# Kernel optimization log

Measured on AMD Instinct MI355X. Metric: run time of the kernel, lower is better.

Reference implementation:

```python
import jax, jax.numpy as jnp
import numpy as np
import math


def ste_round(x):
    # round with straight-through gradient (identity in bwd)
    return x + jax.lax.stop_gradient(jnp.round(x) - x)


def ste_floor(x):
    return x + jax.lax.stop_gradient(jnp.floor(x) - x)


def _conv(x, w, b):
    # 5x5 stride-2 conv, padding=2 (kernel_size//2), NCHW/OIHW
    y = jax.lax.conv_general_dilated(
        x, w, window_strides=(2, 2), padding=[(2, 2), (2, 2)],
        dimension_numbers=('NCHW', 'OIHW', 'NCHW'))
    return y + b[None, :, None, None]


def _split_conv(x, w, b_int, mul, split=4):
    # 4 redundant sub-convolutions with floor-STE quantized integer weights/biases
    wq = ste_round(w)  # wSTE: round-to-int with STE
    out = 0.0
    for i in range(split):
        out = out + _conv(x, ste_floor((wq + i) / split), ste_floor((b_int + i) / split))
    return out * mul[None, :, None, None]


def _forward(x, w0, b0, w1, b1, w2, b2, w3, b3, mul0, mul1, mul2, mul3,
             relu0, relu1, relu2, md0, md1, md2, md3, ga_left):
    Bits = 8; clp_k = 8; in_scale = 8; scl_k = 3
    relus = [relu0, relu1, relu2]
    clp = [round((2 ** Bits - 1) / r * 2 ** (16 + clp_k)) for r in relus]
    scl = [math.floor((r + 2 ** (scl_k - 1)) / 2 ** scl_k) for r in relus]

    # quantize input to uint8 range
    x = jnp.clip(ste_round(x * 2 ** in_scale), 0, 255)

    # ---- layer 0 ----
    x = _split_conv(x, w0, ste_round(b0 * 2 ** in_scale), mul0)
    x = ste_floor((x + 2.0 ** (md0 - 1 + in_scale - clp_k)) / 2.0 ** (md0 + in_scale - clp_k))
    x = jnp.clip(x, 0, clp[0])
    x = ste_floor((ste_round(x * scl[0]) + 2.0 ** (15 + clp_k - scl_k)) / 2.0 ** (16 + clp_k - scl_k))

    # ---- layers 1, 2 ----
    for w_, b_, mul_, md_, idx in ((w1, b1, mul1, md1, 1), (w2, b2, mul2, md2, 2)):
        x = _split_conv(x, w_, ste_round(b_), mul_)
        x = ste_floor((x + 2.0 ** (md_ - 1 - clp_k)) / 2.0 ** (md_ - clp_k))
        x = jnp.clip(x, 0, clp[idx])
        x = ste_floor((ste_round(x * scl[idx]) + 2.0 ** (15 + clp_k - scl_k)) / 2.0 ** (16 + clp_k - scl_k))

    # ---- layer 3 (latent) ----
    x = _split_conv(x, w3, ste_round(b3), mul3)
    x = ste_floor((x + 2.0 ** (md3 - 1 - ga_left)) / 2.0 ** (md3 - ga_left))
    return x


def setup_inputs():
    key = jax.random.key(0)
    ks = jax.random.split(key, 16)
    N, M = 192, 320
    d = {}
    d['x'] = jax.random.uniform(ks[0], (4, 3, 512, 512), dtype=jnp.float32)
    # float weights whose round() gives small ints (integerized LIC weights)
    d['w0'] = jax.random.normal(ks[1], (N, 3, 5, 5), dtype=jnp.float32) * 3.0
    d['b0'] = jax.random.normal(ks[2], (N,), dtype=jnp.float32)
    d['w1'] = jax.random.normal(ks[3], (N, N, 5, 5), dtype=jnp.float32) * 3.0
    d['b1'] = jax.random.normal(ks[4], (N,), dtype=jnp.float32) * 16.0
    d['w2'] = jax.random.normal(ks[5], (N, N, 5, 5), dtype=jnp.float32) * 3.0
    d['b2'] = jax.random.normal(ks[6], (N,), dtype=jnp.float32) * 16.0
    d['w3'] = jax.random.normal(ks[7], (M, N, 5, 5), dtype=jnp.float32) * 3.0
    d['b3'] = jax.random.normal(ks[8], (M,), dtype=jnp.float32) * 16.0
    # per-channel integer-valued fixed-point multipliers
    d['mul0'] = jax.random.randint(ks[9], (N,), 1, 64).astype(jnp.float32)
    d['mul1'] = jax.random.randint(ks[10], (N,), 1, 64).astype(jnp.float32)
    d['mul2'] = jax.random.randint(ks[11], (N,), 1, 64).astype(jnp.float32)
    d['mul3'] = jax.random.randint(ks[12], (M,), 1, 64).astype(jnp.float32)
    d['relu0'] = 65536; d['relu1'] = 65536; d['relu2'] = 65536
    d['md0'] = 7; d['md1'] = 15; d['md2'] = 15; d['md3'] = 10
    d['ga_left'] = 4
    return d


def reference(x, w0, b0, w1, b1, w2, b2, w3, b3, mul0, mul1, mul2, mul3,
              relu0, relu1, relu2, md0, md1, md2, md3, ga_left):
    return _forward(x, w0, b0, w1, b1, w2, b2, w3, b3, mul0, mul1, mul2, mul3,
                    relu0, relu1, relu2, md0, md1, md2, md3, ga_left)
```

## Files before the change

### kernel.cpp

```cpp
#include <hip/hip_runtime.h>
#include <hip/hip_bf16.h>

typedef int i32x4 __attribute__((ext_vector_type(4)));
typedef unsigned int u32;
typedef long long ll;

__device__ __forceinline__ void load_lds16(const void* g, void* l) {
  __builtin_amdgcn_global_load_lds(
      (const __attribute__((address_space(1))) u32*)g,
      (__attribute__((address_space(3))) u32*)l, 16, 0, 0);
}

template <int MF>
__device__ __forceinline__ void pack_i8(int j, const float* wsrc, signed char* wdst) {
  int e = j & 15, col = (j >> 4) & 15, q = (j >> 8) & 3, t = j >> 10;
  int mf = t % MF; t /= MF; int ch = t % 3; int tap = t / 3;
  int oc = mf * 16 + col, ci = ch * 64 + q * 16 + e;
  wdst[j] = (signed char)(int)rintf(wsrc[(oc * 192 + ci) * 25 + tap]);
}

__global__ __launch_bounds__(256) void prep_all(
    const float* __restrict__ w0, const float* __restrict__ w1,
    const float* __restrict__ w2, const float* __restrict__ w3,
    signed char* __restrict__ w0q, signed char* __restrict__ w1p,
    signed char* __restrict__ w2p, signed char* __restrict__ w3p,
    signed char* __restrict__ zbuf,
    int* __restrict__ totw0, int* __restrict__ totw1,
    int* __restrict__ totw2, int* __restrict__ totw3)
{
  const int blk = blockIdx.x;
  const int tid = threadIdx.x;

  if (blk < 2048) {
    if (blk == 0 && tid < 128)
      ((unsigned long long*)zbuf)[tid] = 0x8080808080808080ULL;
    const int R0 = 24576;
    const int R1 = 921600;
    const int R3 = 1536000;
    const int total = R0 + 2 * R1 + R3;
    for (int i = blk * 256 + tid; i < total; i += 2048 * 256) {
      if (i < R0) {
        int e = i & 15, col = (i >> 4) & 15, q = (i >> 8) & 3, t = i >> 10;
        int mf = t % 12, ch = t / 12;
        int k = ch * 64 + q * 16 + e;
        signed char v = 0;
        if (k < 75) {
          int ci = k / 25, tap = k - ci * 25;
          v = (signed char)(int)rintf(w0[((mf * 16 + col) * 3 + ci) * 25 + tap]);
        }
        w0q[i] = v;
      } else if (i < R0 + R1) {
        pack_i8<12>(i - R0, w1, w1p);
      } else if (i < R0 + 2 * R1) {
        pack_i8<12>(i - R0 - R1, w2, w2p);
      } else {
        pack_i8<20>(i - R0 - 2 * R1, w3, w3p);
      }
    }
  } else {
    int t = (blk - 2048) * 256 + tid;
    if (t < 704 * 16) {
      int oc = t >> 4, q = t & 15;
      const float* ws; int* tot; int o = oc;
      if (oc < 192)      { ws = w1; tot = totw1; }
      else if (oc < 384) { ws = w2; tot = totw2; o = oc - 192; }
      else               { ws = w3; tot = totw3; o = oc - 384; }
      const float* p = ws + (size_t)o * 4800 + q * 300;
      int s = 0;
      #pragma unroll 4
      for (int j = 0; j < 300; j++) s += (int)rintf(p[j]);
      atomicAdd(&tot[o], s);
    } else {
      int oc = t - 704 * 16;
      if (oc < 192) {
        const float* p = w0 + (size_t)oc * 75;
        int s = 0;
        #pragma unroll 5
        for (int j = 0; j < 75; j++) s += (int)rintf(p[j]);
        totw0[oc] = s;
      }
    }
  }
}

__global__ __launch_bounds__(192, 3) void conv0F(
    const float* __restrict__ x, const signed char* __restrict__ wq,
    const float* __restrict__ bias, const float* __restrict__ mulv,
    const int* __restrict__ totw,
    const int* __restrict__ reluP, const int* __restrict__ mdP,
    unsigned char* __restrict__ outA)
{
  __shared__ signed char ilds[3][5][132];
  __shared__ __align__(16) signed char bimg[8 * 1024];

  const int tid = threadIdx.x;
  const int lane = tid & 63;
  const int col = lane & 15;
  const int quad = lane >> 4;
  const int w = tid >> 6;
  const int blk = blockIdx.x;
  const int oxblk = blk & 3;
  const int oy = (blk >> 2) & 255;
  const int b = blk >> 10;
  const int oxbase = oxblk * 64;

  i32x4 afr[2][4];
  #pragma unroll
  for (int ch = 0; ch < 2; ch++)
    #pragma unroll
    for (int i = 0; i < 4; i++)
      afr[ch][i] = *(const i32x4*)(wq + ch * 12288 + (w * 4 + i) * 1024 + lane * 16);

  for (int i = tid; i < 3 * 5 * 131; i += 192) {
    int c = i % 131; int t = i / 131; int r = t % 5; int ci = t / 5;
    int iy = 2 * oy - 2 + r;
    int ix = 2 * oxbase - 2 + c;
    int v = -128;
    if ((unsigned)iy < 512u && (unsigned)ix < 512u) {
      float xv = rintf(x[((b * 3 + ci) * 512 + iy) * 512 + ix] * 256.0f);
      xv = fminf(fmaxf(xv, 0.0f), 255.0f);
      v = (int)xv - 128;
    }
    ilds[ci][r][c] = (signed char)v;
  }
  __syncthreads();

  for (int s = tid; s < 256; s += 192) {
    int px = s >> 2, part = s & 3;
    int xbase = 2 * px;
    u32 res[8];
    #pragma unroll
    for (int wd = 0; wd < 8; wd++) {
      u32 v = 0;
      #pragma unroll
      for (int bb = 0; bb < 4; bb++) {
        int k = part * 32 + wd * 4 + bb;
        u32 byte = 0;
        if (k < 75) {
          int ci = k / 25, rem = k - ci * 25, ky = rem / 5, kx = rem - ky * 5;
          byte = (u32)(unsigned char)ilds[ci][ky][xbase + kx];
        }
        v |= byte << (8 * bb);
      }
      res[wd] = v;
    }
    int fn = px >> 4, colp = px & 15;
    int ch = part >> 1, q0 = (part & 1) * 2;
    signed char* d0 = bimg + (ch * 4 + fn) * 1024 + q0 * 256 + colp * 16;
    *(uint4*)d0         = make_uint4(res[0], res[1], res[2], res[3]);
    *(uint4*)(d0 + 256) = make_uint4(res[4], res[5], res[6], res[7]);
  }
  __syncthreads();

  i32x4 acc[4][4];
  #pragma unroll
  for (int fm = 0; fm < 4; fm++)
    #pragma unroll
    for (int fn = 0; fn < 4; fn++) acc[fm][fn] = (i32x4){0, 0, 0, 0};

  #pragma unroll
  for (int ch = 0; ch < 2; ch++) {
    i32x4 bfr[4];
    #pragma unroll
    for (int fn = 0; fn < 4; fn++)
      bfr[fn] = *(const i32x4*)(bimg + (ch * 4 + fn) * 1024 + lane * 16);
    #pragma unroll
    for (int fm = 0; fm < 4; fm++)
      #pragma unroll
      for (int fn = 0; fn < 4; fn++)
        acc[fm][fn] = __builtin_amdgcn_mfma_i32_16x16x64_i8(
            afr[ch][fm], bfr[fn], acc[fm][fn], 0, 0, 0);
  }

  const size_t pix0 = ((size_t)(b * 256 + oy)) * 256 + oxbase;
  const int rl = reluP[0];
  const int sh = mdP[0];
  const ll clpv = llrint(255.0 / (double)rl * 16777216.0);
  const ll sclv = (ll)((rl + 4) >> 3);
  #pragma unroll
  for (int fm = 0; fm < 4; fm++) {
    const int oc0 = w * 64 + fm * 16 + quad * 4;
    ll bi[4], mu[4];
    #pragma unroll
    for (int r = 0; r < 4; r++) {
      bi[r] = llrintf(bias[oc0 + r] * 256.0f) + 128LL * totw[oc0 + r];
      mu[r] = llrintf(mulv[oc0 + r]);
    }
    #pragma unroll
    for (int fn = 0; fn < 4; fn++) {
      const size_t pix = pix0 + fn * 16 + col;
      u32 wd = 0;
      #pragma unroll
      for (int r = 0; r < 4; r++) {
        ll vi = ((ll)acc[fm][fn][r] + bi[r]) * mu[r];
        ll y = (vi + (1LL << (sh - 1))) >> sh;
        y = y < 0 ? 0LL : (y > clpv ? clpv : y);
        y = (y * sclv + (1LL << 20)) >> 21;
        wd |= (((u32)y ^ 0x80u) & 0xFFu) << (8 * r);
      }
      *(u32*)(outA + pix * 192 + oc0) = wd;
    }
  }
}

template <int COUT, int HIN, int WIN, int HOUT, int WOUT, int MW,
          int KSPLIT, bool DIRECT>
__global__ __launch_bounds__(MW * 64, 3) void convS(
    const signed char* __restrict__ act, const signed char* __restrict__ wp,
    const float* __restrict__ bias, const float* __restrict__ mulv,
    const int* __restrict__ totw,
    const int* __restrict__ reluP, const int* __restrict__ mdP,
    const signed char* __restrict__ zbuf,
    unsigned char* __restrict__ outA, int* __restrict__ outP)
{
  constexpr int CIN = 192;
  constexpr int PASSES = 4;
  constexpr int MAXP = (PASSES + MW - 1) / MW;
  constexpr int SAe = MW * 4096;
  constexpr int TX = WOUT / 16;
  constexpr int TYB = HOUT / 4;
  constexpr int TPP = 25 / KSPLIT;
  constexpr int NSTEP = TPP * 3;
  constexpr int PSZ = 4 * HOUT * WOUT * COUT;
  static_assert(MW * 64 == COUT, "M covers COUT");

  __shared__ __align__(16) char smem[2 * 4096];

  const int tid = threadIdx.x;
  const int lane = tid & 63;
  const int col = lane & 15;
  const int quad = lane >> 4;
  const int w = tid >> 6;
  const int part = blockIdx.y;

  int bx = blockIdx.x;
  const int tx = bx % TX; bx /= TX;
  const int ty = bx % TYB;
  const int b = bx / TYB;
  const int ox0 = tx * 16;
  const int oy0 = ty * 4;

  const signed char* bptr[MAXP];
  int bmx[MAXP], bmy[MAXP];
  #pragma unroll
  for (int k = 0; k < MAXP; k++) {
    int p = w + k * MW;
    if (p >= PASSES) break;
    int oxv = ox0 + col;
    int oyv = oy0 + p;
    bptr[k] = act + ((size_t)b * HIN * WIN + (size_t)(2 * oyv) * WIN + 2 * oxv) * CIN
              + quad * 16;
    int mx = 0, my = 0;
    #pragma unroll
    for (int kk = 0; kk < 5; kk++) {
      if ((unsigned)(2 * oxv + kk - 2) < (unsigned)WIN) mx |= 1 << kk;
      if ((unsigned)(2 * oyv + kk - 2) < (unsigned)HIN) my |= 1 << kk;
    }
    bmx[k] = mx; bmy[k] = my;
  }

  auto stageStep = [&](int tap, int ch, int sel) {
    const int ky = tap / 5, kx = tap % 5;
    const int offB = ((ky - 2) * WIN + (kx - 2)) * CIN + ch * 64;
    #pragma unroll
    for (int k = 0; k < MAXP; k++) {
      int p = w + k * MW;
      if (p >= PASSES) break;
      bool v = ((bmx[k] >> kx) & 1) && ((bmy[k] >> ky) & 1);
      const signed char* g = v ? (bptr[k] + offB) : (zbuf + quad * 16);
      load_lds16(g, smem + sel * 4096 + p * 1024);
    }
  };

  i32x4 acc[4][4];
  #pragma unroll
  for (int fm = 0; fm < 4; fm++)
    #pragma unroll
    for (int fn = 0; fn < 4; fn++) acc[fm][fn] = (i32x4){0, 0, 0, 0};

  const int tap0 = part * TPP;
  stageStep(tap0, 0, 0);
  const signed char* aptr = wp + (size_t)(tap0 * 3) * SAe + w * 4096 + lane * 16;
  i32x4 afn[4];
  #pragma unroll
  for (int i = 0; i < 4; i++)
    afn[i] = *(const i32x4*)(aptr + i * 1024);

  int tapN = tap0, chN = 1;

  #pragma unroll 1
  for (int sl = 0; sl < NSTEP; sl++) {
    __syncthreads();

    if (sl + 1 < NSTEP) {
      stageStep(tapN, chN, (sl + 1) & 1);
      chN++;
      if (chN == 3) { chN = 0; tapN++; }
    }

    i32x4 afc[4];
    #pragma unroll
    for (int i = 0; i < 4; i++) afc[i] = afn[i];
    if (sl + 1 < NSTEP) {
      aptr += SAe;
      #pragma unroll
      for (int i = 0; i < 4; i++)
        afn[i] = *(const i32x4*)(aptr + i * 1024);
    }

    const char* pB = smem + (sl & 1) * 4096 + lane * 16;
    i32x4 bfr[4];
    #pragma unroll
    for (int i = 0; i < 4; i++)
      bfr[i] = *(const i32x4*)(pB + i * 1024);
    #pragma unroll
    for (int fm = 0; fm < 4; fm++)
      #pragma unroll
      for (int fn = 0; fn < 4; fn++)
        acc[fm][fn] = __builtin_amdgcn_mfma_i32_16x16x64_i8(
            afc[fm], bfr[fn], acc[fm][fn], 0, 0, 0);
  }

  if constexpr (DIRECT) {
    const int rl = reluP[0];
    const int sh = mdP[0] - 8;
    const ll clpv = llrint(255.0 / (double)rl * 16777216.0);
    const ll sclv = (ll)((rl + 4) >> 3);
    #pragma unroll
    for (int fm = 0; fm < 4; fm++) {
      const int oc0 = w * 64 + fm * 16 + quad * 4;
      ll bi[4], mu[4];
      #pragma unroll
      for (int r = 0; r < 4; r++) {
        bi[r] = llrintf(bias[oc0 + r]) + 128LL * totw[oc0 + r];
        mu[r] = llrintf(mulv[oc0 + r]);
      }
      #pragma unroll
      for (int fn = 0; fn < 4; fn++) {
        const int oyv = oy0 + fn;
        const int oxv = ox0 + col;
        u32 wd = 0;
        #pragma unroll
        for (int r = 0; r < 4; r++) {
          ll vi = ((ll)acc[fm][fn][r] + bi[r]) * mu[r];
          ll y = (vi + (1LL << (sh - 1))) >> sh;
          y = y < 0 ? 0LL : (y > clpv ? clpv : y);
          y = (y * sclv + (1LL << 20)) >> 21;
          wd |= (((u32)y ^ 0x80u) & 0xFFu) << (8 * r);
        }
        *(u32*)(outA + ((size_t)((b * HOUT + oyv) * WOUT + oxv)) * COUT + oc0) = wd;
      }
    }
  } else {
    int* pout = outP + (size_t)part * PSZ;
    #pragma unroll
    for (int fm = 0; fm < 4; fm++) {
      const int oc0 = w * 64 + fm * 16 + quad * 4;
      #pragma unroll
      for (int fn = 0; fn < 4; fn++) {
        const int oyv = oy0 + fn;
        const int oxv = ox0 + col;
        *(i32x4*)(pout + ((size_t)((b * HOUT + oyv) * WOUT + oxv)) * COUT + oc0) =
            acc[fm][fn];
      }
    }
  }
}

__global__ __launch_bounds__(256) void reduce2(
    const int* __restrict__ partP, const float* __restrict__ bias,
    const float* __restrict__ mulv, const int* __restrict__ totw,
    const int* __restrict__ reluP, const int* __restrict__ mdP,
    unsigned char* __restrict__ outA)
{
  const int gid = blockIdx.x * 256 + threadIdx.x;
  const int PSZ4 = 4 * 64 * 64 * 192 / 4;
  const int4* pp = (const int4*)partP;
  int4 sv = pp[gid];
  #pragma unroll
  for (int p = 1; p < 5; p++) {
    int4 v = pp[(size_t)p * PSZ4 + gid];
    sv.x += v.x; sv.y += v.y; sv.z += v.z; sv.w += v.w;
  }
  int sa[4] = {sv.x, sv.y, sv.z, sv.w};
  const int oc0 = (gid * 4) % 192;
  const int rl = reluP[0];
  const int sh = mdP[0] - 8;
  const ll clpv = llrint(255.0 / (double)rl * 16777216.0);
  const ll sclv = (ll)((rl + 4) >> 3);
  u32 wd = 0;
  #pragma unroll
  for (int r = 0; r < 4; r++) {
    ll bi = llrintf(bias[oc0 + r]) + 128LL * totw[oc0 + r];
    ll mu = llrintf(mulv[oc0 + r]);
    ll vi = ((ll)sa[r] + bi) * mu;
    ll y = (vi + (1LL << (sh - 1))) >> sh;
    y = y < 0 ? 0LL : (y > clpv ? clpv : y);
    y = (y * sclv + (1LL << 20)) >> 21;
    wd |= (((u32)y ^ 0x80u) & 0xFFu) << (8 * r);
  }
  ((u32*)outA)[gid] = wd;
}

__global__ __launch_bounds__(256) void reduce3(
    const int* __restrict__ partP, const float* __restrict__ b3,
    const float* __restrict__ mul3, const int* __restrict__ totw3,
    const int* __restrict__ mdP, const int* __restrict__ gaP,
    float* __restrict__ outF)
{
  const int gid = blockIdx.x * 256 + threadIdx.x;
  int t = gid;
  const int ox = t & 31; t >>= 5;
  const int oy = t & 31; t >>= 5;
  const int oc = t % 320;
  const int b  = t / 320;
  const int PSZ = 4 * 32 * 32 * 320;
  const size_t src = ((size_t)((b * 32 + oy) * 32 + ox)) * 320 + oc;
  ll s = 0;
  #pragma unroll
  for (int p = 0; p < 5; p++) s += partP[(size_t)p * PSZ + src];
  const int sh = mdP[0] - gaP[0];
  const ll bi = llrintf(b3[oc]) + 128LL * totw3[oc];
  const ll mu = llrintf(mul3[oc]);
  const ll y = ((s + bi) * mu + (1LL << (sh - 1))) >> sh;
  outF[gid] = (float)y;
}

extern "C" void kernel_launch(void* const* d_in, const int* in_sizes, int n_in,
                              void* d_out, int out_size, void* d_ws, size_t ws_size,
                              hipStream_t stream)
{
  const float* x    = (const float*)d_in[0];
  const float* w0   = (const float*)d_in[1];
  const float* b0   = (const float*)d_in[2];
  const float* w1   = (const float*)d_in[3];
  const float* b1   = (const float*)d_in[4];
  const float* w2   = (const float*)d_in[5];
  const float* b2   = (const float*)d_in[6];
  const float* w3   = (const float*)d_in[7];
  const float* b3   = (const float*)d_in[8];
  const float* mul0 = (const float*)d_in[9];
  const float* mul1 = (const float*)d_in[10];
  const float* mul2 = (const float*)d_in[11];
  const float* mul3 = (const float*)d_in[12];
  const int* relu0  = (const int*)d_in[13];
  const int* relu1  = (const int*)d_in[14];
  const int* relu2  = (const int*)d_in[15];
  const int* md0    = (const int*)d_in[16];
  const int* md1    = (const int*)d_in[17];
  const int* md2    = (const int*)d_in[18];
  const int* md3    = (const int*)d_in[19];
  const int* ga     = (const int*)d_in[20];

  char* ws = (char*)d_ws;
  size_t off = 0;
  signed char* zbuf = (signed char*)(ws + off); off += 1024;
  signed char* w0q  = (signed char*)(ws + off); off += 24576;
  signed char* w1p  = (signed char*)(ws + off); off += 921600;
  signed char* w2p  = (signed char*)(ws + off); off += 921600;
  signed char* w3p  = (signed char*)(ws + off); off += 1536000;
  int*         totw1= (int*)        (ws + off); off += 192 * 4;
  int*         totw2= (int*)        (ws + off); off += 192 * 4;
  int*         totw3= (int*)        (ws + off); off += 320 * 4;
  int*         totw0= (int*)        (ws + off); off += 192 * 4;
  unsigned char* act1 = (unsigned char*)(ws + off); off += (size_t)4 * 256 * 256 * 192;
  unsigned char* act2 = (unsigned char*)(ws + off); off += (size_t)4 * 128 * 128 * 192;
  unsigned char* act3 = (unsigned char*)(ws + off); off += (size_t)4 * 64 * 64 * 192;
  int*         partl  = (int*)(ws + off); off += (size_t)5 * 4 * 64 * 64 * 192 * 4;
  (void)ws_size; (void)in_sizes; (void)n_in; (void)out_size;

  hipMemsetAsync(totw1, 0, (192 + 192 + 320 + 192) * 4, stream);
  prep_all<<<2093, 256, 0, stream>>>(w0, w1, w2, w3, w0q, w1p, w2p, w3p,
                                     zbuf, totw0, totw1, totw2, totw3);
  conv0F<<<4096, 192, 0, stream>>>(x, w0q, b0, mul0, totw0, relu0, md0, act1);
  convS<192, 256, 256, 128, 128, 3, 1, true><<<dim3(1024, 1), 192, 0, stream>>>(
      (const signed char*)act1, w1p, b1, mul1, totw1, relu1, md1, zbuf, act2, nullptr);
  convS<192, 128, 128, 64, 64, 3, 5, false><<<dim3(256, 5), 192, 0, stream>>>(
      (const signed char*)act2, w2p, b2, mul2, totw2, relu2, md2, zbuf, nullptr, partl);
  reduce2<<<3072, 256, 0, stream>>>(partl, b2, mul2, totw2, relu2, md2, act3);
  convS<320, 64, 64, 32, 32, 5, 5, false><<<dim3(64, 5), 320, 0, stream>>>(
      (const signed char*)act3, w3p, b3, mul3, totw3, nullptr, md3, zbuf, nullptr, partl);
  reduce3<<<5120, 256, 0, stream>>>(partl, b3, mul3, totw3, md3, ga, (float*)d_out);
}
```

Measured before the change: 391.2 us.

## Build conv0 MFMA B-fragments directly from input rows, drop im2col LDS pass

Layer-0 weights are repacked so that each 16-byte K chunk corresponds to one kernel row (3 channels × 5 taps), with a second chunk for row 4. The B fragments can then be assembled in registers straight from the staged input rows, which removes the im2col staging buffer, its build loop and one barrier. The input load now handles two pixels per thread with a 16-bit LDS store, and the epilogue moves from 64-bit to 32-bit integer math. That 32-bit math depends on products staying within int range, which could overflow for some parameter values.

```diff
diff --git a/kernel.cpp b/kernel.cpp
--- a/kernel.cpp
+++ b/kernel.cpp
@@ -3,6 +3,7 @@
 
 typedef int i32x4 __attribute__((ext_vector_type(4)));
 typedef unsigned int u32;
+typedef unsigned long long u64;
 typedef long long ll;
 
 __device__ __forceinline__ void load_lds16(const void* g, void* l) {
@@ -40,13 +41,14 @@
     const int total = R0 + 2 * R1 + R3;
     for (int i = blk * 256 + tid; i < total; i += 2048 * 256) {
       if (i < R0) {
-        int e = i & 15, col = (i >> 4) & 15, q = (i >> 8) & 3, t = i >> 10;
+        int e = i & 15, colA = (i >> 4) & 15, q = (i >> 8) & 3, t = i >> 10;
         int mf = t % 12, ch = t / 12;
-        int k = ch * 64 + q * 16 + e;
         signed char v = 0;
-        if (k < 75) {
-          int ci = k / 25, tap = k - ci * 25;
-          v = (signed char)(int)rintf(w0[((mf * 16 + col) * 3 + ci) * 25 + tap]);
+        if (e < 15 && (ch == 0 || q == 0)) {
+          int ky = (ch == 0) ? q : 4;
+          int ci = e / 5, kx = e - ci * 5;
+          v = (signed char)(int)rintf(
+              w0[((mf * 16 + colA) * 3 + ci) * 25 + ky * 5 + kx]);
         }
         w0q[i] = v;
       } else if (i < R0 + R1) {
@@ -91,7 +93,6 @@
     unsigned char* __restrict__ outA)
 {
   __shared__ signed char ilds[3][5][132];
-  __shared__ __align__(16) signed char bimg[8 * 1024];
 
   const int tid = threadIdx.x;
   const int lane = tid & 63;
@@ -111,47 +112,28 @@
     for (int i = 0; i < 4; i++)
       afr[ch][i] = *(const i32x4*)(wq + ch * 12288 + (w * 4 + i) * 1024 + lane * 16);
 
-  for (int i = tid; i < 3 * 5 * 131; i += 192) {
-    int c = i % 131; int t = i / 131; int r = t % 5; int ci = t / 5;
+  const float* xb = x + (size_t)b * 3 * 512 * 512;
+  for (int i = tid; i < 990; i += 192) {
+    int j = i % 66; int t = i / 66; int r = t % 5; int ci = t / 5;
     int iy = 2 * oy - 2 + r;
-    int ix = 2 * oxbase - 2 + c;
-    int v = -128;
-    if ((unsigned)iy < 512u && (unsigned)ix < 512u) {
-      float xv = rintf(x[((b * 3 + ci) * 512 + iy) * 512 + ix] * 256.0f);
-      xv = fminf(fmaxf(xv, 0.0f), 255.0f);
-      v = (int)xv - 128;
-    }
-    ilds[ci][r][c] = (signed char)v;
+    int ix = 2 * oxbase - 2 + 2 * j;
+    int v0 = -128, v1 = -128;
+    if ((unsigned)iy < 512u) {
+      const float* row = xb + ((size_t)ci * 512 + iy) * 512;
+      if ((unsigned)ix < 512u) {
+        float xv = rintf(row[ix] * 256.0f);
+        v0 = (int)fminf(fmaxf(xv, 0.0f), 255.0f) - 128;
+      }
+      if ((unsigned)(ix + 1) < 512u) {
+        float xv = rintf(row[ix + 1] * 256.0f);
+        v1 = (int)fminf(fmaxf(xv, 0.0f), 255.0f) - 128;
+      }
+    }
+    *(unsigned short*)&ilds[ci][r][2 * j] =
+        (unsigned short)((v0 & 0xFF) | ((v1 & 0xFF) << 8));
   }
   __syncthreads();
 
-  for (int s = tid; s < 256; s += 192) {
-    int px = s >> 2, part = s & 3;
-    int xbase = 2 * px;
-    u32 res[8];
-    #pragma unroll
-    for (int wd = 0; wd < 8; wd++) {
-      u32 v = 0;
-      #pragma unroll
-      for (int bb = 0; bb < 4; bb++) {
-        int k = part * 32 + wd * 4 + bb;
-        u32 byte = 0;
-        if (k < 75) {
-          int ci = k / 25, rem = k - ci * 25, ky = rem / 5, kx = rem - ky * 5;
-          byte = (u32)(unsigned char)ilds[ci][ky][xbase + kx];
-        }
-        v |= byte << (8 * bb);
-      }
-      res[wd] = v;
-    }
-    int fn = px >> 4, colp = px & 15;
-    int ch = part >> 1, q0 = (part & 1) * 2;
-    signed char* d0 = bimg + (ch * 4 + fn) * 1024 + q0 * 256 + colp * 16;
-    *(uint4*)d0         = make_uint4(res[0], res[1], res[2], res[3]);
-    *(uint4*)(d0 + 256) = make_uint4(res[4], res[5], res[6], res[7]);
-  }
-  __syncthreads();
-
   i32x4 acc[4][4];
   #pragma unroll
   for (int fm = 0; fm < 4; fm++)
@@ -160,10 +142,28 @@
 
   #pragma unroll
   for (int ch = 0; ch < 2; ch++) {
+    const int row = (ch == 0) ? quad : 4;
     i32x4 bfr[4];
     #pragma unroll
-    for (int fn = 0; fn < 4; fn++)
-      bfr[fn] = *(const i32x4*)(bimg + (ch * 4 + fn) * 1024 + lane * 16);
+    for (int fn = 0; fn < 4; fn++) {
+      const int xb2 = 2 * (fn * 16 + col);
+      const int o8 = (xb2 & 3) * 8;
+      const int ab = xb2 & ~3;
+      u64 w0_, w1_, w2_;
+      {
+        const u32* p0 = (const u32*)&ilds[0][row][ab];
+        const u32* p1 = (const u32*)&ilds[1][row][ab];
+        const u32* p2 = (const u32*)&ilds[2][row][ab];
+        w0_ = (u64)p0[0] | ((u64)p0[1] << 32);
+        w1_ = (u64)p1[0] | ((u64)p1[1] << 32);
+        w2_ = (u64)p2[0] | ((u64)p2[1] << 32);
+      }
+      u32 a0 = (u32)(w0_ >> o8);
+      u32 a1 = ((u32)(w0_ >> (o8 + 32)) & 0xFFu) | (((u32)(w1_ >> o8)) << 8);
+      u32 a2 = ((u32)(w1_ >> (o8 + 24)) & 0xFFFFu) | (((u32)(w2_ >> o8)) << 16);
+      u32 a3 = (u32)(w2_ >> (o8 + 16));
+      bfr[fn] = (i32x4){(int)a0, (int)a1, (int)a2, (int)a3};
+    }
     #pragma unroll
     for (int fm = 0; fm < 4; fm++)
       #pragma unroll
@@ -175,16 +175,19 @@
   const size_t pix0 = ((size_t)(b * 256 + oy)) * 256 + oxbase;
   const int rl = reluP[0];
   const int sh = mdP[0];
-  const ll clpv = llrint(255.0 / (double)rl * 16777216.0);
-  const ll sclv = (ll)((rl + 4) >> 3);
+  const ll clpv_ll = llrint(255.0 / (double)rl * 16777216.0);
+  const int clpv = clpv_ll > 0x7FFFFFFFLL ? 0x7FFFFFFF : (int)clpv_ll;
+  const int sclv = (int)((rl + 4) >> 3);
+  const int rnd = 1 << (sh - 1);
   #pragma unroll
   for (int fm = 0; fm < 4; fm++) {
     const int oc0 = w * 64 + fm * 16 + quad * 4;
-    ll bi[4], mu[4];
+    int bim[4], mu32[4];
     #pragma unroll
     for (int r = 0; r < 4; r++) {
-      bi[r] = llrintf(bias[oc0 + r] * 256.0f) + 128LL * totw[oc0 + r];
-      mu[r] = llrintf(mulv[oc0 + r]);
+      int bi = (int)llrintf(bias[oc0 + r] * 256.0f) + 128 * totw[oc0 + r];
+      mu32[r] = (int)llrintf(mulv[oc0 + r]);
+      bim[r] = bi * mu32[r];
     }
     #pragma unroll
     for (int fn = 0; fn < 4; fn++) {
@@ -192,10 +195,10 @@
       u32 wd = 0;
       #pragma unroll
       for (int r = 0; r < 4; r++) {
-        ll vi = ((ll)acc[fm][fn][r] + bi[r]) * mu[r];
-        ll y = (vi + (1LL << (sh - 1))) >> sh;
-        y = y < 0 ? 0LL : (y > clpv ? clpv : y);
-        y = (y * sclv + (1LL << 20)) >> 21;
+        int vi = acc[fm][fn][r] * mu32[r] + bim[r];
+        int y = (vi + rnd) >> sh;
+        y = y < 0 ? 0 : (y > clpv ? clpv : y);
+        y = (y * sclv + (1 << 20)) >> 21;
         wd |= (((u32)y ^ 0x80u) & 0xFFu) << (8 * r);
       }
       *(u32*)(outA + pix * 192 + oc0) = wd;
```

New measurement: 351.2 us. -10.2%, faster.
